# Performance work log

Hardware: AMD Instinct MI355X
Metric: run time of the kernel (lower is better)

## Reference

```python
import jax, jax.numpy as jnp
import numpy as np

ETYPES = ((0, 2), (4, 6))  # per-metapath edge-type indices into the doubled r_vec table
ALPHA = 3.0


def celu3(x):
    return jax.nn.celu(x, alpha=ALPHA)


def cmul(a, b):
    # complex multiply, last dim = (real, imag)
    re = a[..., 0] * b[..., 0] - a[..., 1] * b[..., 1]
    im = a[..., 0] * b[..., 1] + a[..., 1] * b[..., 0]
    return jnp.stack([re, im], axis=-1)


def setup_inputs() -> dict:
    key = jax.random.key(0)
    ks = jax.random.split(key, 10)
    N, H, heads, M, E, P = 50000, 64, 4, 2, 250000, 3
    R, FH = 4, 128
    D = heads * H
    return {
        "features": jax.random.normal(ks[0], (N, H), jnp.float32),
        "r_vec": jax.random.normal(ks[1], (R, H // 2, 2), jnp.float32),
        "attn1_w": jax.random.normal(ks[2], (heads, H), jnp.float32) * 0.1,
        "attn2": jax.random.normal(ks[3], (1, heads, H), jnp.float32) * 0.1,
        "fw1": jax.random.normal(ks[4], (2 * FH, D), jnp.float32) * 0.05,
        "fb1": jnp.zeros((2 * FH,), jnp.float32),
        "fw2": jax.random.normal(ks[5], (FH, 2 * FH), jnp.float32) * 0.05,
        "fb2": jnp.zeros((FH,), jnp.float32),
        "fw3": jax.random.normal(ks[6], (1, FH), jnp.float32) * 0.05,
        "instances": jax.random.randint(ks[7], (M, E, P), 0, N, jnp.int32),
    }


def reference(features, r_vec, attn1_w, attn2, fw1, fb1, fw2, fb2, fw3, instances):
    N, H = features.shape
    M, E, P = instances.shape
    heads = attn1_w.shape[0]
    # unit-modulus rotations + conjugates: [2R, H/2, 2], even=r, odd=conj(r)
    rv = r_vec / jnp.linalg.norm(r_vec, axis=2, keepdims=True)
    conj = rv * jnp.array([1.0, -1.0], rv.dtype)
    rv2 = jnp.stack([rv, conj], axis=1).reshape(-1, H // 2, 2)

    per_path = []
    for m in range(M):
        inst = instances[m]  # [E, P]
        # backward cumulative rotation: final_r[i] = prod_{j>=i} r_{etype[j]}, final_r[P-1]=1
        ident = jnp.stack([jnp.ones(H // 2, rv.dtype), jnp.zeros(H // 2, rv.dtype)], axis=-1)
        frs = [ident]
        for i in range(P - 2, -1, -1):
            frs.insert(0, cmul(frs[0], rv2[ETYPES[m][i]]))
        fr = jnp.stack(frs)  # [P, H/2, 2]
        # gather features along metapath and rotate (last position rotated by identity)
        edata = features[inst].reshape(E, P, H // 2, 2)
        rot = cmul(edata, fr[None])
        me = jnp.mean(rot.reshape(E, P, H), axis=1)  # [E, H]
        se = celu3(me) * jax.nn.sigmoid(me)  # gated metapath embedding
        eft = celu3(se)  # same across heads in original (tiled)
        seg = inst[:, 0]  # target node per instance
        a1 = celu3(features[seg] @ attn1_w.T)  # [E, heads]
        a2 = jnp.einsum('eh,kh->ek', eft, attn2[0])  # [E, heads]
        a = celu3(a1 + a2)
        # segment softmax over each node's instance set
        amax = jax.ops.segment_max(a, seg, num_segments=N)
        ex = jnp.exp(a - amax[seg])
        den = jax.ops.segment_sum(ex, seg, num_segments=N)
        attn = ex / den[seg]  # [E, heads]
        hsum = jax.ops.segment_sum(attn[:, :, None] * eft[:, None, :], seg, num_segments=N)
        per_path.append(celu3(hsum).reshape(N, heads * H))  # empty nodes -> 0

    z = jnp.stack(per_path, axis=1)  # [N, M, D]
    t = celu3(z @ fw1.T + fb1)
    t = celu3(t @ fw2.T + fb2)
    w = (t @ fw3.T).mean(axis=0)  # [M, 1]
    beta = jax.nn.softmax(w, axis=0)
    out = (beta * z).sum(axis=1)  # [N, D]
    return out
```

## Files before the change

kernel.cpp:

```cpp
#include <hip/hip_runtime.h>
#include <hip/hip_bf16.h>

typedef unsigned short u16;
typedef unsigned int   u32;
typedef short bf16x8 __attribute__((ext_vector_type(8)));
typedef float f32x4  __attribute__((ext_vector_type(4)));

#define CAP 64

__device__ inline float b2f(u16 u){ return __builtin_bit_cast(float, (u32)u << 16); }
__device__ inline u16 f2b(float f){
  u32 x = __builtin_bit_cast(u32, f);
  x += 0x7fffu + ((x >> 16) & 1u);
  return (u16)(x >> 16);
}
__device__ inline u32 pk2(float lo, float hi){
  float2 f; f.x = lo; f.y = hi;
  __hip_bfloat162 h = __float22bfloat162_rn(f);
  u32 r; __builtin_memcpy(&r, &h, 4);
  return r;
}
__device__ inline void up2(u32 u, float& lo, float& hi){
  lo = __builtin_bit_cast(float, u << 16);
  hi = __builtin_bit_cast(float, u & 0xffff0000u);
}
__device__ inline float fexp(float x){ return __expf(x); }
__device__ inline float frcp(float x){ return __builtin_amdgcn_rcpf(x); }
__device__ inline float celu3(float x){
  return x > 0.f ? x : 3.f * (__expf(x * (1.f/3.f)) - 1.f);
}
__device__ inline float act_chain(float x){
  float u  = __expf(x * (1.f/3.f));
  float u3 = u*u*u;
  float sg = u3 * frcp(u3 + 1.f);
  float c1 = x > 0.f ? x : 3.f*u - 3.f;
  float se = c1 * sg;
  return se > 0.f ? se : 3.f*__expf(se*(1.f/3.f)) - 3.f;
}

__global__ __launch_bounds__(256) void pre_kernel(
    const float* __restrict__ feat, const float* __restrict__ attn1,
    const float* __restrict__ rvec, const float* __restrict__ fw1,
    const float* __restrict__ fw2,
    u16* __restrict__ featb, u16* __restrict__ rotA, u16* __restrict__ rotB,
    float* __restrict__ a1c, u16* __restrict__ fw1b, u16* __restrict__ fw2b,
    int* __restrict__ cnt, float* __restrict__ wacc,
    int N, int nbA)
{
  __shared__ float w1s[256], rvs[256];
  int b = blockIdx.x, t = threadIdx.x;
  if (b >= nbA){
    int cb = b - nbA;
    if (cb < 48){
      const float* src = (cb < 32) ? fw1 : fw2;
      u16* dst = (cb < 32) ? fw1b : fw2b;
      int i = (cb < 32 ? cb : cb - 32)*256 + t;
      float4 a = ((const float4*)src)[2*i], bb = ((const float4*)src)[2*i + 1];
      uint4 o;
      o.x = pk2(a.x, a.y);  o.y = pk2(a.z, a.w);
      o.z = pk2(bb.x, bb.y); o.w = pk2(bb.z, bb.w);
      ((uint4*)dst)[i] = o;
      return;
    }
    cb -= 48;
    int i = cb*256 + t;
    if (i*4 < 2*N) ((uint4*)cnt)[i] = make_uint4(0u,0u,0u,0u);
    if (cb == 0 && t < 128) wacc[t] = 0.f;
    return;
  }
  w1s[t] = attn1[t];
  rvs[t] = rvec[t];
  __syncthreads();
  int g = t >> 4, l = t & 15;
  int n = b * 16 + g;
  if (n >= N) return;
  float4 x = ((const float4*)feat)[(size_t)n*16 + l];
  float4 xs;
  xs.x = x.x*(1.f/3.f); xs.y = x.y*(1.f/3.f);
  xs.z = x.z*(1.f/3.f); xs.w = x.w*(1.f/3.f);
  uint2 o;
  o.x = pk2(xs.x, xs.y);
  o.y = pk2(xs.z, xs.w);
  ((uint2*)featb)[(size_t)n*16 + l] = o;

  #pragma unroll
  for (int m = 0; m < 2; ++m){
    float4 ra = *(const float4*)&rvs[(2*m)*64 + l*4];
    float4 rb = *(const float4*)&rvs[(2*m+1)*64 + l*4];
    float na0 = rsqrtf(ra.x*ra.x + ra.y*ra.y); ra.x*=na0; ra.y*=na0;
    float na1 = rsqrtf(ra.z*ra.z + ra.w*ra.w); ra.z*=na1; ra.w*=na1;
    float nb0 = rsqrtf(rb.x*rb.x + rb.y*rb.y); rb.x*=nb0; rb.y*=nb0;
    float nb1 = rsqrtf(rb.z*rb.z + rb.w*rb.w); rb.z*=nb1; rb.w*=nb1;
    float A0r = rb.x*ra.x - rb.y*ra.y, A0i = rb.x*ra.y + rb.y*ra.x;
    float A1r = rb.z*ra.z - rb.w*ra.w, A1i = rb.z*ra.w + rb.w*ra.z;
    uint2 oa, ob;
    oa.x = pk2(xs.x*A0r - xs.y*A0i, xs.x*A0i + xs.y*A0r);
    oa.y = pk2(xs.z*A1r - xs.w*A1i, xs.z*A1i + xs.w*A1r);
    ob.x = pk2(xs.x*rb.x - xs.y*rb.y, xs.x*rb.y + xs.y*rb.x);
    ob.y = pk2(xs.z*rb.z - xs.w*rb.w, xs.z*rb.w + xs.w*rb.z);
    ((uint2*)rotA)[((size_t)m*N + n)*16 + l] = oa;
    ((uint2*)rotB)[((size_t)m*N + n)*16 + l] = ob;
  }

  float d[4];
  #pragma unroll
  for (int k = 0; k < 4; ++k){
    int wb = k*64 + l*4;
    d[k] = x.x*w1s[wb] + x.y*w1s[wb+1] + x.z*w1s[wb+2] + x.w*w1s[wb+3];
  }
  #pragma unroll
  for (int off = 8; off; off >>= 1){
    #pragma unroll
    for (int k = 0; k < 4; ++k) d[k] += __shfl_xor(d[k], off);
  }
  if (l == 0){
    float4 av;
    av.x = celu3(d[0]); av.y = celu3(d[1]);
    av.z = celu3(d[2]); av.w = celu3(d[3]);
    ((float4*)a1c)[n] = av;
  }
}

__global__ __launch_bounds__(256) void edge_kernel(
    const u16* __restrict__ rotA, const u16* __restrict__ rotB,
    const u16* __restrict__ featb, const int* __restrict__ inst,
    const float* __restrict__ a1c, const float* __restrict__ attn2,
    u16* __restrict__ eft, float* __restrict__ a_ws,
    int* __restrict__ cnt, int* __restrict__ bucket, int E, int N)
{
  __shared__ float w2s[256];
  int m = blockIdx.y;
  int t = threadIdx.x;
  w2s[t] = attn2[t];
  __syncthreads();

  int g = t >> 3, l = t & 7;
  int e0 = blockIdx.x * 64 + g;
  int e1 = e0 + 32;
  bool ok0 = e0 < E, ok1 = e1 < E;
  int ec0 = ok0 ? e0 : 0, ec1 = ok1 ? e1 : 0;
  size_t mN = (size_t)m * N;
  size_t mE = (size_t)m * E;

  int b0 = (int)((mE + ec0)*3), b1 = (int)((mE + ec1)*3);
  int i00 = inst[b0], i01 = inst[b0+1], i02 = inst[b0+2];
  int i10 = inst[b1], i11 = inst[b1+1], i12 = inst[b1+2];

  uint4 v00 = ((const uint4*)rotA)[(mN + i00)*8 + l];
  uint4 v01 = ((const uint4*)rotB)[(mN + i01)*8 + l];
  uint4 v02 = ((const uint4*)featb)[(size_t)i02*8 + l];
  uint4 v10 = ((const uint4*)rotA)[(mN + i10)*8 + l];
  uint4 v11 = ((const uint4*)rotB)[(mN + i11)*8 + l];
  uint4 v12 = ((const uint4*)featb)[(size_t)i12*8 + l];

  float A[8], B[8], C[8], ef0[8], ef1[8];
  up2(v00.x, A[0], A[1]); up2(v00.y, A[2], A[3]);
  up2(v00.z, A[4], A[5]); up2(v00.w, A[6], A[7]);
  up2(v01.x, B[0], B[1]); up2(v01.y, B[2], B[3]);
  up2(v01.z, B[4], B[5]); up2(v01.w, B[6], B[7]);
  up2(v02.x, C[0], C[1]); up2(v02.y, C[2], C[3]);
  up2(v02.z, C[4], C[5]); up2(v02.w, C[6], C[7]);
  #pragma unroll
  for (int c = 0; c < 8; ++c) ef0[c] = act_chain(A[c] + B[c] + C[c]);

  up2(v10.x, A[0], A[1]); up2(v10.y, A[2], A[3]);
  up2(v10.z, A[4], A[5]); up2(v10.w, A[6], A[7]);
  up2(v11.x, B[0], B[1]); up2(v11.y, B[2], B[3]);
  up2(v11.z, B[4], B[5]); up2(v11.w, B[6], B[7]);
  up2(v12.x, C[0], C[1]); up2(v12.y, C[2], C[3]);
  up2(v12.z, C[4], C[5]); up2(v12.w, C[6], C[7]);
  #pragma unroll
  for (int c = 0; c < 8; ++c) ef1[c] = act_chain(A[c] + B[c] + C[c]);

  if (ok0){
    uint4 uo;
    uo.x = pk2(ef0[0], ef0[1]); uo.y = pk2(ef0[2], ef0[3]);
    uo.z = pk2(ef0[4], ef0[5]); uo.w = pk2(ef0[6], ef0[7]);
    ((uint4*)eft)[(mE + e0)*8 + l] = uo;
  }
  if (ok1){
    uint4 uo;
    uo.x = pk2(ef1[0], ef1[1]); uo.y = pk2(ef1[2], ef1[3]);
    uo.z = pk2(ef1[4], ef1[5]); uo.w = pk2(ef1[6], ef1[7]);
    ((uint4*)eft)[(mE + e1)*8 + l] = uo;
  }

  float d20[4], d21[4];
  #pragma unroll
  for (int k = 0; k < 4; ++k){
    int wb = k*64 + l*8;
    float4 wA = *(const float4*)&w2s[wb];
    float4 wB = *(const float4*)&w2s[wb+4];
    d20[k] = ef0[0]*wA.x + ef0[1]*wA.y + ef0[2]*wA.z + ef0[3]*wA.w
           + ef0[4]*wB.x + ef0[5]*wB.y + ef0[6]*wB.z + ef0[7]*wB.w;
    d21[k] = ef1[0]*wA.x + ef1[1]*wA.y + ef1[2]*wA.z + ef1[3]*wA.w
           + ef1[4]*wB.x + ef1[5]*wB.y + ef1[6]*wB.z + ef1[7]*wB.w;
  }
  #pragma unroll
  for (int off = 4; off; off >>= 1){
    #pragma unroll
    for (int k = 0; k < 4; ++k){
      d20[k] += __shfl_xor(d20[k], off);
      d21[k] += __shfl_xor(d21[k], off);
    }
  }
  if (l == 0){
    if (ok0){
      float4 a1v4 = ((const float4*)a1c)[i00];
      float4 av;
      av.x = celu3(a1v4.x + d20[0]);
      av.y = celu3(a1v4.y + d20[1]);
      av.z = celu3(a1v4.z + d20[2]);
      av.w = celu3(a1v4.w + d20[3]);
      ((float4*)a_ws)[mE + e0] = av;
      int pos = atomicAdd(&cnt[m*N + i00], 1);
      if (pos < CAP) bucket[(size_t)(m*N + i00)*CAP + pos] = e0;
    }
    if (ok1){
      float4 a1v4 = ((const float4*)a1c)[i10];
      float4 av;
      av.x = celu3(a1v4.x + d21[0]);
      av.y = celu3(a1v4.y + d21[1]);
      av.z = celu3(a1v4.z + d21[2]);
      av.w = celu3(a1v4.w + d21[3]);
      ((float4*)a_ws)[mE + e1] = av;
      int pos = atomicAdd(&cnt[m*N + i10], 1);
      if (pos < CAP) bucket[(size_t)(m*N + i10)*CAP + pos] = e1;
    }
  }
}

__global__ __launch_bounds__(256) void seg_kernel(
    const float* __restrict__ a_ws, const u16* __restrict__ eft,
    const int* __restrict__ cnt, const int* __restrict__ bucket,
    u16* __restrict__ z, int E, int N)
{
  __shared__ float wls[4][64][4];
  __shared__ int   els[4][64];
  int wvb = threadIdx.x >> 6;
  int m = blockIdx.y;
  int n = blockIdx.x * 4 + wvb;
  if (n >= N) return;
  int lane = threadIdx.x & 63;
  int sidx = m*N + n;
  int deg = cnt[sidx]; if (deg > CAP) deg = CAP;

  float h0=0.f, h1=0.f, h2=0.f, h3=0.f;
  if (deg > 0){
    const int* bk = bucket + (size_t)sidx * CAP;
    size_t ebase = (size_t)m * E;

    int e = (lane < deg) ? bk[lane] : 0;
    float w0 = 0.f, w1 = 0.f, w2 = 0.f, w3 = 0.f;
    if (lane < deg){
      float4 av = ((const float4*)a_ws)[ebase + e];
      w0 = fexp(av.x); w1 = fexp(av.y); w2 = fexp(av.z); w3 = fexp(av.w);
    }
    els[wvb][lane] = e;
    *(float4*)&wls[wvb][lane][0] = make_float4(w0, w1, w2, w3);

    float d0=w0, d1=w1, d2=w2, d3=w3;
    #pragma unroll
    for (int off = 32; off; off >>= 1){
      d0 += __shfl_xor(d0, off); d1 += __shfl_xor(d1, off);
      d2 += __shfl_xor(d2, off); d3 += __shfl_xor(d3, off);
    }

    const u16* ep = eft + ebase*64 + lane;
    int j = 0;
    for (; j + 3 < deg; j += 4){
      int ej0 = els[wvb][j],   ej1 = els[wvb][j+1];
      int ej2 = els[wvb][j+2], ej3 = els[wvb][j+3];
      float ev0 = b2f(ep[(size_t)ej0*64]);
      float ev1 = b2f(ep[(size_t)ej1*64]);
      float ev2 = b2f(ep[(size_t)ej2*64]);
      float ev3 = b2f(ep[(size_t)ej3*64]);
      float4 wj0 = *(const float4*)&wls[wvb][j][0];
      float4 wj1 = *(const float4*)&wls[wvb][j+1][0];
      float4 wj2 = *(const float4*)&wls[wvb][j+2][0];
      float4 wj3 = *(const float4*)&wls[wvb][j+3][0];
      h0 += wj0.x*ev0; h1 += wj0.y*ev0; h2 += wj0.z*ev0; h3 += wj0.w*ev0;
      h0 += wj1.x*ev1; h1 += wj1.y*ev1; h2 += wj1.z*ev1; h3 += wj1.w*ev1;
      h0 += wj2.x*ev2; h1 += wj2.y*ev2; h2 += wj2.z*ev2; h3 += wj2.w*ev2;
      h0 += wj3.x*ev3; h1 += wj3.y*ev3; h2 += wj3.z*ev3; h3 += wj3.w*ev3;
    }
    for (; j < deg; ++j){
      int ej0 = els[wvb][j];
      float4 wj0 = *(const float4*)&wls[wvb][j][0];
      float ev0 = b2f(ep[(size_t)ej0*64]);
      h0 += wj0.x*ev0; h1 += wj0.y*ev0; h2 += wj0.z*ev0; h3 += wj0.w*ev0;
    }
    h0 *= frcp(d0); h1 *= frcp(d1); h2 *= frcp(d2); h3 *= frcp(d3);
  }
  u16* zr = z + (size_t)sidx*256 + lane;
  zr[0]   = f2b(celu3(h0));
  zr[64]  = f2b(celu3(h1));
  zr[128] = f2b(celu3(h2));
  zr[192] = f2b(celu3(h3));
}

__global__ __launch_bounds__(512, 2) void mlp_kernel(
    const u16* __restrict__ z, const u16* __restrict__ fw1b, const float* __restrict__ fb1,
    const u16* __restrict__ fw2b, const float* __restrict__ fb2, const float* __restrict__ fw3,
    float* __restrict__ waccP, int rows, int N)
{
  __shared__ u16 buf[64][264];
  __shared__ float fw3s[128];
  __shared__ float sPart[8][64];
  int tid = threadIdx.x;
  int wv = tid >> 6, lane = tid & 63, lr = lane & 15, quad = lane >> 4;
  f32x4 zero4 = {0.f, 0.f, 0.f, 0.f};

  const u16* wb1 = fw1b + (size_t)(wv*32 + lr)*256 + quad*8;
  bf16x8 B1[2][8];
  #pragma unroll
  for (int nt = 0; nt < 2; ++nt)
    #pragma unroll
    for (int ks = 0; ks < 8; ++ks)
      B1[nt][ks] = *(const bf16x8*)(wb1 + nt*16*256 + ks*32);
  #pragma unroll
  for (int nt = 0; nt < 2; ++nt)
    #pragma unroll
    for (int ks = 0; ks < 8; ++ks)
      asm volatile("" :: "v"(B1[nt][ks]));

  const u16* wb2 = fw2b + (size_t)(wv*16 + lr)*256 + quad*8;
  if (tid < 128) fw3s[tid] = fw3[tid];

  const uint4* zg = (const uint4*)z;
  int ntiles = (rows + 63) >> 6;
  int gstride = gridDim.x;
  int tile = blockIdx.x;

  uint4 zr4[4];
  {
    int row0 = tile * 64;
    #pragma unroll
    for (int it = 0; it < 4; ++it){
      int idx = it*512 + tid;
      int row = idx >> 5, c8 = idx & 31;
      int gr = row0 + row;
      zr4[it] = make_uint4(0u,0u,0u,0u);
      if (gr < rows) zr4[it] = zg[(size_t)gr*32 + c8];
    }
  }

  for (; tile < ntiles; ){
    int row0 = tile * 64;
    #pragma unroll
    for (int it = 0; it < 4; ++it){
      int idx = it*512 + tid;
      int row = idx >> 5, c8 = idx & 31;
      *(uint4*)&buf[row][c8*8] = zr4[it];
    }
    __syncthreads();

    int tnext = tile + gstride;
    uint4 zn[4];
    {
      int nrow0 = tnext * 64;
      #pragma unroll
      for (int it = 0; it < 4; ++it){
        int idx = it*512 + tid;
        int row = idx >> 5, c8 = idx & 31;
        int gr = nrow0 + row;
        zn[it] = make_uint4(0u,0u,0u,0u);
        if (tnext < ntiles && gr < rows) zn[it] = zg[(size_t)gr*32 + c8];
      }
    }

    f32x4 acc[4][2];
    #pragma unroll
    for (int a = 0; a < 4; ++a){ acc[a][0] = zero4; acc[a][1] = zero4; }
    #pragma unroll
    for (int ks = 0; ks < 8; ++ks){
      #pragma unroll
      for (int mt = 0; mt < 4; ++mt){
        bf16x8 af = *(const bf16x8*)&buf[mt*16 + lr][ks*32 + quad*8];
        acc[mt][0] = __builtin_amdgcn_mfma_f32_16x16x32_bf16(af, B1[0][ks], acc[mt][0], 0, 0, 0);
        acc[mt][1] = __builtin_amdgcn_mfma_f32_16x16x32_bf16(af, B1[1][ks], acc[mt][1], 0, 0, 0);
      }
    }

    bf16x8 B2[8];
    #pragma unroll
    for (int ks = 0; ks < 8; ++ks)
      B2[ks] = *(const bf16x8*)(wb2 + ks*32);

    __syncthreads();
    #pragma unroll
    for (int nt = 0; nt < 2; ++nt){
      int col = wv*32 + nt*16 + lr;
      float bias = fb1[col];
      #pragma unroll
      for (int mt = 0; mt < 4; ++mt)
        #pragma unroll
        for (int ri = 0; ri < 4; ++ri){
          int row = mt*16 + quad*4 + ri;
          buf[row][col] = f2b(celu3(acc[mt][nt][ri] + bias));
        }
    }
    __syncthreads();

    f32x4 acc2[4];
    #pragma unroll
    for (int a = 0; a < 4; ++a) acc2[a] = zero4;
    #pragma unroll
    for (int ks = 0; ks < 8; ++ks){
      #pragma unroll
      for (int mt = 0; mt < 4; ++mt){
        bf16x8 af = *(const bf16x8*)&buf[mt*16 + lr][ks*32 + quad*8];
        acc2[mt] = __builtin_amdgcn_mfma_f32_16x16x32_bf16(af, B2[ks], acc2[mt], 0, 0, 0);
      }
    }

    {
      int col = wv*16 + lr;
      float bias2 = fb2[col];
      float w3 = fw3s[col];
      float ps[4][4];
      #pragma unroll
      for (int mt = 0; mt < 4; ++mt)
        #pragma unroll
        for (int ri = 0; ri < 4; ++ri)
          ps[mt][ri] = celu3(acc2[mt][ri] + bias2) * w3;
      #pragma unroll
      for (int off = 8; off; off >>= 1)
        #pragma unroll
        for (int mt = 0; mt < 4; ++mt)
          #pragma unroll
          for (int ri = 0; ri < 4; ++ri)
            ps[mt][ri] += __shfl_xor(ps[mt][ri], off);
      if (lr == 0){
        #pragma unroll
        for (int mt = 0; mt < 4; ++mt)
          #pragma unroll
          for (int ri = 0; ri < 4; ++ri)
            sPart[wv][mt*16 + quad*4 + ri] = ps[mt][ri];
      }
    }
    __syncthreads();

    if (tid < 64){
      float s = 0.f;
      #pragma unroll
      for (int w = 0; w < 8; ++w) s += sPart[w][tid];
      int gr = row0 + tid;
      if (gr >= rows) s = 0.f;
      float s0 = (gr < N) ? s : 0.f;
      float s1 = (gr < N) ? 0.f : s;
      #pragma unroll
      for (int off = 32; off; off >>= 1){
        s0 += __shfl_xor(s0, off);
        s1 += __shfl_xor(s1, off);
      }
      if (tid == 0){
        int slot = tile & 63;
        atomicAdd(&waccP[slot],      s0);
        atomicAdd(&waccP[64 + slot], s1);
      }
    }

    #pragma unroll
    for (int it = 0; it < 4; ++it) zr4[it] = zn[it];
    tile = tnext;
  }
}

__global__ __launch_bounds__(256) void out_kernel(
    const u16* __restrict__ z, const float* __restrict__ wacc,
    float* __restrict__ out, int total, float invN)
{
  __shared__ float bsh[2];
  int tid = threadIdx.x;
  if (tid < 64){
    float s0 = wacc[tid], s1 = wacc[64 + tid];
    #pragma unroll
    for (int off = 32; off; off >>= 1){
      s0 += __shfl_xor(s0, off);
      s1 += __shfl_xor(s1, off);
    }
    if (tid == 0){
      float w0 = s0*invN, w1 = s1*invN;
      float mx = fmaxf(w0, w1);
      float e0 = __expf(w0 - mx), e1 = __expf(w1 - mx);
      float s = e0 + e1;
      bsh[0] = e0 / s;
      bsh[1] = e1 / s;
    }
  }
  __syncthreads();
  float b0 = bsh[0], b1 = bsh[1];
  int idx = blockIdx.x * 256 + tid;
  if (idx*8 >= total) return;
  uint4 u0 = ((const uint4*)z)[idx];
  uint4 u1 = ((const uint4*)z)[(total >> 3) + idx];
  float a0,a1v,c0,c1;
  float4 o;
  up2(u0.x, a0, a1v); up2(u1.x, c0, c1);
  o.x = b0*a0 + b1*c0; o.y = b0*a1v + b1*c1;
  up2(u0.y, a0, a1v); up2(u1.y, c0, c1);
  o.z = b0*a0 + b1*c0; o.w = b0*a1v + b1*c1;
  ((float4*)out)[idx*2] = o;
  up2(u0.z, a0, a1v); up2(u1.z, c0, c1);
  o.x = b0*a0 + b1*c0; o.y = b0*a1v + b1*c1;
  up2(u0.w, a0, a1v); up2(u1.w, c0, c1);
  o.z = b0*a0 + b1*c0; o.w = b0*a1v + b1*c1;
  ((float4*)out)[idx*2 + 1] = o;
}

extern "C" void kernel_launch(void* const* d_in, const int* in_sizes, int n_in,
                              void* d_out, int out_size, void* d_ws, size_t ws_size,
                              hipStream_t stream)
{
  (void)n_in; (void)out_size; (void)ws_size;
  const float* feat  = (const float*)d_in[0];
  const float* rvec  = (const float*)d_in[1];
  const float* attn1 = (const float*)d_in[2];
  const float* attn2 = (const float*)d_in[3];
  const float* fw1   = (const float*)d_in[4];
  const float* fb1   = (const float*)d_in[5];
  const float* fw2   = (const float*)d_in[6];
  const float* fb2   = (const float*)d_in[7];
  const float* fw3   = (const float*)d_in[8];
  const int*   inst  = (const int*)d_in[9];

  int N = in_sizes[0] / 64;
  int E = in_sizes[9] / 6;

  char* ws = (char*)d_ws;
  u16*   z      = (u16*)ws;                            size_t zB = (size_t)2*N*256*2;
  u16*   eft    = (u16*)(ws + zB);                     size_t eB = (size_t)2*E*64*2;
  float* a_ws   = (float*)(ws + zB + eB);              size_t aB = (size_t)2*E*4*4;
  int*   bucket = (int*)(ws + zB + eB + aB);           size_t bB = (size_t)2*N*CAP*4;
  int*   cnt    = (int*)(ws + zB + eB + aB + bB);      size_t cB = (size_t)2*N*4;
  u16*   featb  = (u16*)(ws + zB + eB + aB + bB + cB); size_t fB = (size_t)N*64*2;
  float* a1c    = (float*)(ws + zB + eB + aB + bB + cB + fB);  size_t a1B = (size_t)N*4*4;
  u16*   fw1b   = (u16*)(ws + zB + eB + aB + bB + cB + fB + a1B);
  u16*   fw2b   = fw1b + 256*256;
  float* wacc   = (float*)(fw2b + 128*256);

  u16* rotA = z;
  u16* rotB = z + (size_t)2*N*64;

  int nbA = (N + 15)/16;
  int nbZ = ((2*N)/4 + 255)/256;
  pre_kernel<<<nbA + 48 + nbZ, 256, 0, stream>>>(
      feat, attn1, rvec, fw1, fw2, featb, rotA, rotB, a1c, fw1b, fw2b,
      cnt, wacc, N, nbA);
  edge_kernel<<<dim3((E + 63)/64, 2), 256, 0, stream>>>(
      rotA, rotB, featb, inst, a1c, attn2, eft, a_ws, cnt, bucket, E, N);
  seg_kernel<<<dim3((N + 3)/4, 2), 256, 0, stream>>>(a_ws, eft, cnt, bucket, z, E, N);
  mlp_kernel<<<512, 512, 0, stream>>>(z, fw1b, fb1, fw2b, fb2, fw3, wacc, 2*N, N);
  out_kernel<<<((N*256/8) + 255)/256, 256, 0, stream>>>(z, wacc, (float*)d_out, N*256, 1.f/(float)N);
}
```

Measured before the change: 266.8 us.

## Process two segments per wave in seg_kernel and approximate second celu

The segment aggregation kernel now assigns a 32-lane half-wave to each node instead of a full wave. Each lane loads a packed pair of bf16 eft values and writes packed bf16x2 outputs, which halves the number of waves and uses wider memory accesses. Separately, the second celu in the activation chain is replaced by a quadratic polynomial for negative inputs, removing one exp per element. That polynomial only approximates the exponential and is accurate only for small-magnitude negative values.

```diff
diff --git a/kernel.cpp b/kernel.cpp
--- a/kernel.cpp
+++ b/kernel.cpp
@@ -29,13 +29,13 @@
 __device__ inline float celu3(float x){
   return x > 0.f ? x : 3.f * (__expf(x * (1.f/3.f)) - 1.f);
 }
-__device__ inline float act_chain(float x){
+__device__ inline float act1(float x){
   float u  = __expf(x * (1.f/3.f));
   float u3 = u*u*u;
   float sg = u3 * frcp(u3 + 1.f);
   float c1 = x > 0.f ? x : 3.f*u - 3.f;
   float se = c1 * sg;
-  return se > 0.f ? se : 3.f*__expf(se*(1.f/3.f)) - 3.f;
+  return se > 0.f ? se : se + se*se*(1.f/6.f);
 }
 
 __global__ __launch_bounds__(256) void pre_kernel(
@@ -161,7 +161,7 @@
   up2(v02.x, C[0], C[1]); up2(v02.y, C[2], C[3]);
   up2(v02.z, C[4], C[5]); up2(v02.w, C[6], C[7]);
   #pragma unroll
-  for (int c = 0; c < 8; ++c) ef0[c] = act_chain(A[c] + B[c] + C[c]);
+  for (int c = 0; c < 8; ++c) ef0[c] = act1(A[c] + B[c] + C[c]);
 
   up2(v10.x, A[0], A[1]); up2(v10.y, A[2], A[3]);
   up2(v10.z, A[4], A[5]); up2(v10.w, A[6], A[7]);
@@ -170,7 +170,7 @@
   up2(v12.x, C[0], C[1]); up2(v12.y, C[2], C[3]);
   up2(v12.z, C[4], C[5]); up2(v12.w, C[6], C[7]);
   #pragma unroll
-  for (int c = 0; c < 8; ++c) ef1[c] = act_chain(A[c] + B[c] + C[c]);
+  for (int c = 0; c < 8; ++c) ef1[c] = act1(A[c] + B[c] + C[c]);
 
   if (ok0){
     uint4 uo;
@@ -235,68 +235,84 @@
     const int* __restrict__ cnt, const int* __restrict__ bucket,
     u16* __restrict__ z, int E, int N)
 {
-  __shared__ float wls[4][64][4];
-  __shared__ int   els[4][64];
-  int wvb = threadIdx.x >> 6;
+  __shared__ float wls[8][64][4];
+  __shared__ int   els[8][64];
+  int tid = threadIdx.x;
+  int wvb = tid >> 6;
+  int lane = tid & 63;
+  int half = lane >> 5, l = lane & 31;
+  int seg = wvb*2 + half;
   int m = blockIdx.y;
-  int n = blockIdx.x * 4 + wvb;
-  if (n >= N) return;
-  int lane = threadIdx.x & 63;
-  int sidx = m*N + n;
-  int deg = cnt[sidx]; if (deg > CAP) deg = CAP;
-
-  float h0=0.f, h1=0.f, h2=0.f, h3=0.f;
-  if (deg > 0){
-    const int* bk = bucket + (size_t)sidx * CAP;
-    size_t ebase = (size_t)m * E;
-
-    int e = (lane < deg) ? bk[lane] : 0;
-    float w0 = 0.f, w1 = 0.f, w2 = 0.f, w3 = 0.f;
-    if (lane < deg){
-      float4 av = ((const float4*)a_ws)[ebase + e];
-      w0 = fexp(av.x); w1 = fexp(av.y); w2 = fexp(av.z); w3 = fexp(av.w);
-    }
-    els[wvb][lane] = e;
-    *(float4*)&wls[wvb][lane][0] = make_float4(w0, w1, w2, w3);
-
-    float d0=w0, d1=w1, d2=w2, d3=w3;
-    #pragma unroll
-    for (int off = 32; off; off >>= 1){
-      d0 += __shfl_xor(d0, off); d1 += __shfl_xor(d1, off);
-      d2 += __shfl_xor(d2, off); d3 += __shfl_xor(d3, off);
-    }
-
-    const u16* ep = eft + ebase*64 + lane;
-    int j = 0;
-    for (; j + 3 < deg; j += 4){
-      int ej0 = els[wvb][j],   ej1 = els[wvb][j+1];
-      int ej2 = els[wvb][j+2], ej3 = els[wvb][j+3];
-      float ev0 = b2f(ep[(size_t)ej0*64]);
-      float ev1 = b2f(ep[(size_t)ej1*64]);
-      float ev2 = b2f(ep[(size_t)ej2*64]);
-      float ev3 = b2f(ep[(size_t)ej3*64]);
-      float4 wj0 = *(const float4*)&wls[wvb][j][0];
-      float4 wj1 = *(const float4*)&wls[wvb][j+1][0];
-      float4 wj2 = *(const float4*)&wls[wvb][j+2][0];
-      float4 wj3 = *(const float4*)&wls[wvb][j+3][0];
-      h0 += wj0.x*ev0; h1 += wj0.y*ev0; h2 += wj0.z*ev0; h3 += wj0.w*ev0;
-      h0 += wj1.x*ev1; h1 += wj1.y*ev1; h2 += wj1.z*ev1; h3 += wj1.w*ev1;
-      h0 += wj2.x*ev2; h1 += wj2.y*ev2; h2 += wj2.z*ev2; h3 += wj2.w*ev2;
-      h0 += wj3.x*ev3; h1 += wj3.y*ev3; h2 += wj3.z*ev3; h3 += wj3.w*ev3;
-    }
-    for (; j < deg; ++j){
-      int ej0 = els[wvb][j];
-      float4 wj0 = *(const float4*)&wls[wvb][j][0];
-      float ev0 = b2f(ep[(size_t)ej0*64]);
-      h0 += wj0.x*ev0; h1 += wj0.y*ev0; h2 += wj0.z*ev0; h3 += wj0.w*ev0;
-    }
-    h0 *= frcp(d0); h1 *= frcp(d1); h2 *= frcp(d2); h3 *= frcp(d3);
-  }
-  u16* zr = z + (size_t)sidx*256 + lane;
-  zr[0]   = f2b(celu3(h0));
-  zr[64]  = f2b(celu3(h1));
-  zr[128] = f2b(celu3(h2));
-  zr[192] = f2b(celu3(h3));
+  int n = blockIdx.x * 8 + seg;
+  bool valid = n < N;
+  int sidx = m*N + (valid ? n : 0);
+  int deg = 0;
+  if (valid){ deg = cnt[sidx]; deg = deg > CAP ? CAP : deg; }
+  size_t ebase = (size_t)m * E;
+  const int* bk = bucket + (size_t)sidx * CAP;
+
+  float w0a=0.f,w1a=0.f,w2a=0.f,w3a=0.f, w0b=0.f,w1b=0.f,w2b=0.f,w3b=0.f;
+  int ea = 0, eb = 0;
+  if (l < deg){
+    ea = bk[l];
+    float4 av = ((const float4*)a_ws)[ebase + ea];
+    w0a=fexp(av.x); w1a=fexp(av.y); w2a=fexp(av.z); w3a=fexp(av.w);
+  }
+  if (l + 32 < deg){
+    eb = bk[l+32];
+    float4 av = ((const float4*)a_ws)[ebase + eb];
+    w0b=fexp(av.x); w1b=fexp(av.y); w2b=fexp(av.z); w3b=fexp(av.w);
+  }
+  els[seg][l]    = ea;
+  els[seg][l+32] = eb;
+  *(float4*)&wls[seg][l][0]    = make_float4(w0a,w1a,w2a,w3a);
+  *(float4*)&wls[seg][l+32][0] = make_float4(w0b,w1b,w2b,w3b);
+
+  float d0=w0a+w0b, d1=w1a+w1b, d2=w2a+w2b, d3=w3a+w3b;
+  #pragma unroll
+  for (int off = 16; off; off >>= 1){
+    d0 += __shfl_xor(d0, off); d1 += __shfl_xor(d1, off);
+    d2 += __shfl_xor(d2, off); d3 += __shfl_xor(d3, off);
+  }
+
+  float hA0=0.f,hA1=0.f,hA2=0.f,hA3=0.f;
+  float hB0=0.f,hB1=0.f,hB2=0.f,hB3=0.f;
+  const u32* ep = (const u32*)eft;
+  int j = 0;
+  for (; j + 1 < deg; j += 2){
+    int ej0 = els[seg][j], ej1 = els[seg][j+1];
+    u32 p0 = ep[(ebase + ej0)*32 + l];
+    u32 p1 = ep[(ebase + ej1)*32 + l];
+    float4 wj0 = *(const float4*)&wls[seg][j][0];
+    float4 wj1 = *(const float4*)&wls[seg][j+1][0];
+    float eva, evb;
+    up2(p0, eva, evb);
+    hA0 += wj0.x*eva; hA1 += wj0.y*eva; hA2 += wj0.z*eva; hA3 += wj0.w*eva;
+    hB0 += wj0.x*evb; hB1 += wj0.y*evb; hB2 += wj0.z*evb; hB3 += wj0.w*evb;
+    up2(p1, eva, evb);
+    hA0 += wj1.x*eva; hA1 += wj1.y*eva; hA2 += wj1.z*eva; hA3 += wj1.w*eva;
+    hB0 += wj1.x*evb; hB1 += wj1.y*evb; hB2 += wj1.z*evb; hB3 += wj1.w*evb;
+  }
+  if (j < deg){
+    int ej0 = els[seg][j];
+    u32 p0 = ep[(ebase + ej0)*32 + l];
+    float4 wj0 = *(const float4*)&wls[seg][j][0];
+    float eva, evb;
+    up2(p0, eva, evb);
+    hA0 += wj0.x*eva; hA1 += wj0.y*eva; hA2 += wj0.z*eva; hA3 += wj0.w*eva;
+    hB0 += wj0.x*evb; hB1 += wj0.y*evb; hB2 += wj0.z*evb; hB3 += wj0.w*evb;
+  }
+  float r0 = deg > 0 ? frcp(d0) : 0.f;
+  float r1 = deg > 0 ? frcp(d1) : 0.f;
+  float r2 = deg > 0 ? frcp(d2) : 0.f;
+  float r3 = deg > 0 ? frcp(d3) : 0.f;
+  if (valid){
+    u32* zr = (u32*)(z + (size_t)sidx*256) + l;
+    zr[0]  = pk2(celu3(hA0*r0), celu3(hB0*r0));
+    zr[32] = pk2(celu3(hA1*r1), celu3(hB1*r1));
+    zr[64] = pk2(celu3(hA2*r2), celu3(hB2*r2));
+    zr[96] = pk2(celu3(hA3*r3), celu3(hB3*r3));
+  }
 }
 
 __global__ __launch_bounds__(512, 2) void mlp_kernel(
@@ -550,7 +566,7 @@
       cnt, wacc, N, nbA);
   edge_kernel<<<dim3((E + 63)/64, 2), 256, 0, stream>>>(
       rotA, rotB, featb, inst, a1c, attn2, eft, a_ws, cnt, bucket, E, N);
-  seg_kernel<<<dim3((N + 3)/4, 2), 256, 0, stream>>>(a_ws, eft, cnt, bucket, z, E, N);
+  seg_kernel<<<dim3((N + 7)/8, 2), 256, 0, stream>>>(a_ws, eft, cnt, bucket, z, E, N);
   mlp_kernel<<<512, 512, 0, stream>>>(z, fw1b, fb1, fw2b, fb2, fw3, wacc, 2*N, N);
   out_kernel<<<((N*256/8) + 255)/256, 256, 0, stream>>>(z, wacc, (float*)d_out, N*256, 1.f/(float)N);
 }
```

Result: faster. 249.5 us (-6.5%).
